# Optimization experiments

Measured on AMD Instinct MI355X. Metric: run time of the kernel, lower is better.

Reference implementation:

```python
import jax, jax.numpy as jnp
import numpy as np

B = 8          # number of point clouds
P = 2048       # points per cloud (equal-length segments)
D_FEAT = 16    # matched feature dim
BIG = 1e10     # mask value for cross-batch pairs

LOSS_WEIGHT = 1.0
COORD_WEIGHT = 1.0
FEAT_WEIGHT = 0.1


def setup_inputs() -> dict:
    key = jax.random.key(0)
    k1, k2, k3, k4 = jax.random.split(key, 4)
    n = B * P
    pred_coord = jax.random.normal(k1, (n, 3), dtype=jnp.float32) * 10.0
    target_coord = jax.random.normal(k2, (n, 3), dtype=jnp.float32) * 10.0
    pred_feat = jax.random.normal(k3, (n, D_FEAT), dtype=jnp.float32)
    target_feat = jax.random.normal(k4, (n, D_FEAT), dtype=jnp.float32)
    offsets = (jnp.arange(1, B + 1) * P).astype(jnp.int32)  # cumulative ends
    return {
        'pred_coord': pred_coord,
        'target_coord': target_coord,
        'pred_feat': pred_feat,
        'target_feat': target_feat,
        'pred_offset': offsets,
        'target_offset': offsets,
    }


def _batch_ids(offsets, n):
    # point i belongs to batch b where offsets[b-1] <= i < offsets[b]
    return jnp.searchsorted(offsets, jnp.arange(n), side='right')


def _lengths(offsets):
    prev = jnp.concatenate([jnp.zeros((1,), offsets.dtype), offsets[:-1]])
    return offsets - prev


def _nn_dist(x, y, xb, yb):
    # masked all-pairs squared distances [n, m]; per-batch KNN(k=1)
    d2 = (jnp.sum(x * x, axis=1)[:, None]
          - 2.0 * (x @ y.T)
          + jnp.sum(y * y, axis=1)[None, :])
    d2 = jnp.where(xb[:, None] == yb[None, :], d2, BIG)
    idx = jnp.argmin(d2, axis=1)
    nearest = y[idx]                          # gather nearest neighbor
    dist = jnp.sum((x - nearest) ** 2, axis=1)  # norm=2, recomputed as in torch
    return dist, idx


def _chamfer_dir(x, y, x_off, y_off):
    xb = _batch_ids(x_off, x.shape[0])
    yb = _batch_ids(y_off, y.shape[0])
    dist, idx = _nn_dist(x, y, xb, yb)
    seg = jax.ops.segment_sum(dist, xb, num_segments=B)
    lens = jnp.maximum(_lengths(x_off), 1).astype(dist.dtype)
    return seg / lens, idx                    # point_reduction='mean'


def reference(pred_coord, target_coord, pred_feat, target_feat,
              pred_offset, target_offset):
    cham_x, x_idx = _chamfer_dir(pred_coord, target_coord, pred_offset, target_offset)
    cham_y, _ = _chamfer_dir(target_coord, pred_coord, target_offset, pred_offset)
    # bidirectional sum, batch_reduction='mean' (weights None -> divide by B)
    coord_loss = jnp.sum(cham_x + cham_y) / B
    # matched feature MSE via pred->target nearest-neighbor indices
    nearest_feat = target_feat[x_idx]
    feat_loss = jnp.mean((pred_feat - nearest_feat) ** 2)
    loss = LOSS_WEIGHT * (COORD_WEIGHT * coord_loss + FEAT_WEIGHT * feat_loss)
    return (loss, coord_loss, feat_loss)
```

## Files before the change

kernel.cpp:

```cpp
#include <hip/hip_runtime.h>

#define BATCHES 8
#define PTS     2048
#define DFEAT   16
#define NQ      16384
#define NKEY    (2 * NQ)

__global__ __launch_bounds__(512, 4) void
nn_kernel(const float* __restrict__ pred_coord,
          const float* __restrict__ target_coord,
          unsigned long long* __restrict__ keys) {
    __shared__ float4 cand[512];
    __shared__ unsigned long long pk[8][256];

    const int bid     = blockIdx.x;
    const int dir     = bid >> 8;
    const int rem     = bid & 255;
    const int batch   = rem >> 5;
    const int qg      = (rem >> 2) & 7;
    const int quarter = rem & 3;
    const int tid     = threadIdx.x;
    const int lane    = tid & 63;
    const int wv      = tid >> 6;

    const float* x = (dir == 0) ? pred_coord   : target_coord;
    const float* y = (dir == 0) ? target_coord : pred_coord;

    const float* ybase = y + ((size_t)batch * PTS + quarter * 512) * 3;
    {
        int k = tid;
        float cx = ybase[3 * k], cy = ybase[3 * k + 1], cz = ybase[3 * k + 2];
        cand[k] = make_float4(cx, cy, cz, 0.5f * (cx * cx + cy * cy + cz * cz));
    }
    __syncthreads();

    const int qbase = batch * PTS + qg * 256;
    float nax[4], nay[4], naz[4], hx[4];
    #pragma unroll
    for (int k = 0; k < 4; ++k) {
        int q = qbase + lane + 64 * k;
        float ax = x[3 * q], ay = x[3 * q + 1], az = x[3 * q + 2];
        nax[k] = -ax; nay[k] = -ay; naz[k] = -az;
        hx[k]  = 0.5f * (ax * ax + ay * ay + az * az);
    }

    const int jbase = wv * 64;
    float best[4] = {1e30f, 1e30f, 1e30f, 1e30f};
    int   bj[4]   = {0, 0, 0, 0};
    if (dir == 0) {
        #pragma unroll 8
        for (int i = 0; i < 64; ++i) {
            int j = jbase + i;
            float4 c = cand[j];
            #pragma unroll
            for (int k = 0; k < 4; ++k) {
                float s = fmaf(nax[k], c.x,
                          fmaf(nay[k], c.y,
                          fmaf(naz[k], c.z, c.w)));
                if (s < best[k]) { best[k] = s; bj[k] = j; }
            }
        }
    } else {
        #pragma unroll 8
        for (int i = 0; i < 64; ++i) {
            float4 c = cand[jbase + i];
            #pragma unroll
            for (int k = 0; k < 4; ++k) {
                float s = fmaf(nax[k], c.x,
                          fmaf(nay[k], c.y,
                          fmaf(naz[k], c.z, c.w)));
                best[k] = fminf(best[k], s);
            }
        }
    }
    const unsigned int goff = quarter * 512;
    #pragma unroll
    for (int k = 0; k < 4; ++k) {
        pk[wv][lane + 64 * k] =
            ((unsigned long long)__float_as_uint(fmaxf(best[k] + hx[k], 0.f)) << 32)
            | (goff + (unsigned int)bj[k]);
    }
    __syncthreads();

    if (tid < 256) {
        unsigned long long m = pk[0][tid];
        #pragma unroll
        for (int c = 1; c < 8; ++c) {
            unsigned long long v = pk[c][tid];
            m = (v < m) ? v : m;
        }
        keys[(size_t)quarter * NKEY + (size_t)dir * NQ + qbase + tid] = m;
    }
}

__global__ __launch_bounds__(256) void
merge_kernel(const float* __restrict__ pred_feat,
             const float* __restrict__ target_feat,
             const unsigned long long* __restrict__ keys,
             float2* __restrict__ partials) {
    __shared__ float wa[4], wb[4];
    const int t   = blockIdx.x * 256 + threadIdx.x;
    const int dir = t >> 14;
    const int q   = t & (NQ - 1);
    const int batch = q >> 11;

    unsigned long long m = keys[t];
    #pragma unroll
    for (int qq = 1; qq < 4; ++qq) {
        unsigned long long v = keys[(size_t)qq * NKEY + t];
        m = (v < m) ? v : m;
    }

    float ds = 2.0f * __uint_as_float((unsigned int)(m >> 32));
    float fs = 0.f;
    if (dir == 0) {
        const int row = batch * PTS + (int)(m & 0xffffffffu);
        const float4* pf = (const float4*)(pred_feat + (size_t)q * DFEAT);
        const float4* tf = (const float4*)(target_feat + (size_t)row * DFEAT);
        #pragma unroll
        for (int k = 0; k < 4; ++k) {
            float4 a = pf[k], b = tf[k];
            float d0 = a.x - b.x, d1 = a.y - b.y, d2 = a.z - b.z, d3 = a.w - b.w;
            fs += d0 * d0 + d1 * d1 + d2 * d2 + d3 * d3;
        }
    }

    #pragma unroll
    for (int off = 32; off > 0; off >>= 1) {
        ds += __shfl_down(ds, off);
        fs += __shfl_down(fs, off);
    }
    const int wave = threadIdx.x >> 6, lane = threadIdx.x & 63;
    if (lane == 0) { wa[wave] = ds; wb[wave] = fs; }
    __syncthreads();
    if (threadIdx.x == 0) {
        partials[blockIdx.x] = make_float2(wa[0] + wa[1] + wa[2] + wa[3],
                                           wb[0] + wb[1] + wb[2] + wb[3]);
    }
}

__global__ __launch_bounds__(128) void
final_kernel(const float2* __restrict__ partials, float* __restrict__ out) {
    __shared__ float a[2], b[2];
    const int tid = threadIdx.x;
    float2 p = partials[tid];
    float ds = p.x, fs = p.y;
    #pragma unroll
    for (int off = 32; off > 0; off >>= 1) {
        ds += __shfl_down(ds, off);
        fs += __shfl_down(fs, off);
    }
    const int wave = tid >> 6, lane = tid & 63;
    if (lane == 0) { a[wave] = ds; b[wave] = fs; }
    __syncthreads();
    if (tid == 0) {
        float dsum = a[0] + a[1];
        float fsum = b[0] + b[1];
        float coord_loss = dsum / (float)(BATCHES * PTS);
        float feat_loss  = fsum / (float)(NQ * DFEAT);
        out[0] = coord_loss + 0.1f * feat_loss;
        out[1] = coord_loss;
        out[2] = feat_loss;
    }
}

extern "C" void kernel_launch(void* const* d_in, const int* in_sizes, int n_in,
                              void* d_out, int out_size, void* d_ws, size_t ws_size,
                              hipStream_t stream) {
    const float* pred_coord   = (const float*)d_in[0];
    const float* target_coord = (const float*)d_in[1];
    const float* pred_feat    = (const float*)d_in[2];
    const float* target_feat  = (const float*)d_in[3];

    unsigned long long* keys = (unsigned long long*)d_ws;
    float2* partials = (float2*)((char*)d_ws + 4ull * NKEY * sizeof(unsigned long long));

    nn_kernel<<<512, 512, 0, stream>>>(pred_coord, target_coord, keys);
    merge_kernel<<<128, 256, 0, stream>>>(pred_feat, target_feat, keys, partials);
    final_kernel<<<1, 128, 0, stream>>>(partials, (float*)d_out);
}
```

Before: 76.06 us.

## Fuse NN search with merge and feature loss, full-batch candidates per block

Each block now loads all 2048 candidates of its batch into shared memory and handles 64 queries, with the 8 waves splitting the candidate range. The cross-wave argmin, the distance sum and the matched feature MSE are done inside the same kernel, so the intermediate key buffer and the separate merge kernel launch go away. The cost is that each thread keeps only one query instead of four, which lowers register-level reuse of candidate loads from LDS, and each block uses more shared memory.

```diff
diff --git a/kernel.cpp b/kernel.cpp
--- a/kernel.cpp
+++ b/kernel.cpp
@@ -4,125 +4,95 @@
 #define PTS     2048
 #define DFEAT   16
 #define NQ      16384
-#define NKEY    (2 * NQ)
+#define NBLK    512
 
 __global__ __launch_bounds__(512, 4) void
-nn_kernel(const float* __restrict__ pred_coord,
-          const float* __restrict__ target_coord,
-          unsigned long long* __restrict__ keys) {
-    __shared__ float4 cand[512];
-    __shared__ unsigned long long pk[8][256];
+nn_fused_kernel(const float* __restrict__ pred_coord,
+                const float* __restrict__ target_coord,
+                const float* __restrict__ pred_feat,
+                const float* __restrict__ target_feat,
+                float2* __restrict__ partials) {
+    __shared__ float4 cand[2048];
+    __shared__ unsigned long long pk[8][64];
+    __shared__ unsigned long long fk[64];
+    __shared__ float wa[8], wb[8];
 
-    const int bid     = blockIdx.x;
-    const int dir     = bid >> 8;
-    const int rem     = bid & 255;
-    const int batch   = rem >> 5;
-    const int qg      = (rem >> 2) & 7;
-    const int quarter = rem & 3;
-    const int tid     = threadIdx.x;
-    const int lane    = tid & 63;
-    const int wv      = tid >> 6;
+    const int bid   = blockIdx.x;
+    const int dir   = bid >> 8;
+    const int rem   = bid & 255;
+    const int batch = rem >> 5;
+    const int qg    = rem & 31;
+    const int tid   = threadIdx.x;
+    const int lane  = tid & 63;
+    const int slice = tid >> 6;
 
     const float* x = (dir == 0) ? pred_coord   : target_coord;
     const float* y = (dir == 0) ? target_coord : pred_coord;
 
-    const float* ybase = y + ((size_t)batch * PTS + quarter * 512) * 3;
-    {
-        int k = tid;
+    const float* ybase = y + (size_t)batch * PTS * 3;
+    #pragma unroll
+    for (int r = 0; r < 4; ++r) {
+        int k = tid + 512 * r;
         float cx = ybase[3 * k], cy = ybase[3 * k + 1], cz = ybase[3 * k + 2];
         cand[k] = make_float4(cx, cy, cz, 0.5f * (cx * cx + cy * cy + cz * cz));
     }
+
+    const int qbase = batch * PTS + qg * 64;
+    const int q = qbase + lane;
+    float ax = x[3 * q], ay = x[3 * q + 1], az = x[3 * q + 2];
+    const float nax = -ax, nay = -ay, naz = -az;
+    const float hx  = 0.5f * (ax * ax + ay * ay + az * az);
+
     __syncthreads();
 
-    const int qbase = batch * PTS + qg * 256;
-    float nax[4], nay[4], naz[4], hx[4];
-    #pragma unroll
-    for (int k = 0; k < 4; ++k) {
-        int q = qbase + lane + 64 * k;
-        float ax = x[3 * q], ay = x[3 * q + 1], az = x[3 * q + 2];
-        nax[k] = -ax; nay[k] = -ay; naz[k] = -az;
-        hx[k]  = 0.5f * (ax * ax + ay * ay + az * az);
-    }
-
-    const int jbase = wv * 64;
-    float best[4] = {1e30f, 1e30f, 1e30f, 1e30f};
-    int   bj[4]   = {0, 0, 0, 0};
+    const int jbase = slice * 256;
+    float best = 1e30f;
+    int   bj   = 0;
     if (dir == 0) {
         #pragma unroll 8
-        for (int i = 0; i < 64; ++i) {
-            int j = jbase + i;
-            float4 c = cand[j];
-            #pragma unroll
-            for (int k = 0; k < 4; ++k) {
-                float s = fmaf(nax[k], c.x,
-                          fmaf(nay[k], c.y,
-                          fmaf(naz[k], c.z, c.w)));
-                if (s < best[k]) { best[k] = s; bj[k] = j; }
-            }
+        for (int i = 0; i < 256; ++i) {
+            float4 c = cand[jbase + i];
+            float s = fmaf(nax, c.x,
+                      fmaf(nay, c.y,
+                      fmaf(naz, c.z, c.w)));
+            if (s < best) { best = s; bj = i; }
         }
     } else {
         #pragma unroll 8
-        for (int i = 0; i < 64; ++i) {
+        for (int i = 0; i < 256; ++i) {
             float4 c = cand[jbase + i];
-            #pragma unroll
-            for (int k = 0; k < 4; ++k) {
-                float s = fmaf(nax[k], c.x,
-                          fmaf(nay[k], c.y,
-                          fmaf(naz[k], c.z, c.w)));
-                best[k] = fminf(best[k], s);
-            }
+            float s = fmaf(nax, c.x,
+                      fmaf(nay, c.y,
+                      fmaf(naz, c.z, c.w)));
+            best = fminf(best, s);
         }
     }
-    const unsigned int goff = quarter * 512;
-    #pragma unroll
-    for (int k = 0; k < 4; ++k) {
-        pk[wv][lane + 64 * k] =
-            ((unsigned long long)__float_as_uint(fmaxf(best[k] + hx[k], 0.f)) << 32)
-            | (goff + (unsigned int)bj[k]);
-    }
+    pk[slice][lane] =
+        ((unsigned long long)__float_as_uint(fmaxf(best + hx, 0.f)) << 32)
+        | (unsigned int)(jbase + bj);
     __syncthreads();
 
-    if (tid < 256) {
+    float ds = 0.f, fs = 0.f;
+    if (tid < 64) {
         unsigned long long m = pk[0][tid];
         #pragma unroll
         for (int c = 1; c < 8; ++c) {
             unsigned long long v = pk[c][tid];
             m = (v < m) ? v : m;
         }
-        keys[(size_t)quarter * NKEY + (size_t)dir * NQ + qbase + tid] = m;
+        fk[tid] = m;
+        ds = 2.0f * __uint_as_float((unsigned int)(m >> 32));
     }
-}
+    __syncthreads();
 
-__global__ __launch_bounds__(256) void
-merge_kernel(const float* __restrict__ pred_feat,
-             const float* __restrict__ target_feat,
-             const unsigned long long* __restrict__ keys,
-             float2* __restrict__ partials) {
-    __shared__ float wa[4], wb[4];
-    const int t   = blockIdx.x * 256 + threadIdx.x;
-    const int dir = t >> 14;
-    const int q   = t & (NQ - 1);
-    const int batch = q >> 11;
-
-    unsigned long long m = keys[t];
-    #pragma unroll
-    for (int qq = 1; qq < 4; ++qq) {
-        unsigned long long v = keys[(size_t)qq * NKEY + t];
-        m = (v < m) ? v : m;
-    }
-
-    float ds = 2.0f * __uint_as_float((unsigned int)(m >> 32));
-    float fs = 0.f;
-    if (dir == 0) {
+    if (dir == 0 && tid < 256) {
+        const unsigned long long m = fk[tid >> 2];
         const int row = batch * PTS + (int)(m & 0xffffffffu);
-        const float4* pf = (const float4*)(pred_feat + (size_t)q * DFEAT);
+        const float4* pf = (const float4*)(pred_feat + (size_t)(qbase + (tid >> 2)) * DFEAT);
         const float4* tf = (const float4*)(target_feat + (size_t)row * DFEAT);
-        #pragma unroll
-        for (int k = 0; k < 4; ++k) {
-            float4 a = pf[k], b = tf[k];
-            float d0 = a.x - b.x, d1 = a.y - b.y, d2 = a.z - b.z, d3 = a.w - b.w;
-            fs += d0 * d0 + d1 * d1 + d2 * d2 + d3 * d3;
-        }
+        float4 a = pf[tid & 3], b = tf[tid & 3];
+        float d0 = a.x - b.x, d1 = a.y - b.y, d2 = a.z - b.z, d3 = a.w - b.w;
+        fs = d0 * d0 + d1 * d1 + d2 * d2 + d3 * d3;
     }
 
     #pragma unroll
@@ -130,18 +100,19 @@
         ds += __shfl_down(ds, off);
         fs += __shfl_down(fs, off);
     }
-    const int wave = threadIdx.x >> 6, lane = threadIdx.x & 63;
-    if (lane == 0) { wa[wave] = ds; wb[wave] = fs; }
+    if (lane == 0) { wa[slice] = ds; wb[slice] = fs; }
     __syncthreads();
-    if (threadIdx.x == 0) {
-        partials[blockIdx.x] = make_float2(wa[0] + wa[1] + wa[2] + wa[3],
-                                           wb[0] + wb[1] + wb[2] + wb[3]);
+    if (tid == 0) {
+        float a = 0.f, b = 0.f;
+        #pragma unroll
+        for (int w = 0; w < 8; ++w) { a += wa[w]; b += wb[w]; }
+        partials[bid] = make_float2(a, b);
     }
 }
 
-__global__ __launch_bounds__(128) void
+__global__ __launch_bounds__(512) void
 final_kernel(const float2* __restrict__ partials, float* __restrict__ out) {
-    __shared__ float a[2], b[2];
+    __shared__ float a8[8], b8[8];
     const int tid = threadIdx.x;
     float2 p = partials[tid];
     float ds = p.x, fs = p.y;
@@ -151,11 +122,12 @@
         fs += __shfl_down(fs, off);
     }
     const int wave = tid >> 6, lane = tid & 63;
-    if (lane == 0) { a[wave] = ds; b[wave] = fs; }
+    if (lane == 0) { a8[wave] = ds; b8[wave] = fs; }
     __syncthreads();
     if (tid == 0) {
-        float dsum = a[0] + a[1];
-        float fsum = b[0] + b[1];
+        float dsum = 0.f, fsum = 0.f;
+        #pragma unroll
+        for (int w = 0; w < 8; ++w) { dsum += a8[w]; fsum += b8[w]; }
         float coord_loss = dsum / (float)(BATCHES * PTS);
         float feat_loss  = fsum / (float)(NQ * DFEAT);
         out[0] = coord_loss + 0.1f * feat_loss;
@@ -172,10 +144,9 @@
     const float* pred_feat    = (const float*)d_in[2];
     const float* target_feat  = (const float*)d_in[3];
 
-    unsigned long long* keys = (unsigned long long*)d_ws;
-    float2* partials = (float2*)((char*)d_ws + 4ull * NKEY * sizeof(unsigned long long));
+    float2* partials = (float2*)d_ws;
 
-    nn_kernel<<<512, 512, 0, stream>>>(pred_coord, target_coord, keys);
-    merge_kernel<<<128, 256, 0, stream>>>(pred_feat, target_feat, keys, partials);
-    final_kernel<<<1, 128, 0, stream>>>(partials, (float*)d_out);
+    nn_fused_kernel<<<NBLK, 512, 0, stream>>>(pred_coord, target_coord,
+                                              pred_feat, target_feat, partials);
+    final_kernel<<<1, 512, 0, stream>>>(partials, (float*)d_out);
 }
```

New measurement: 88.91 us. 16.9% more time.
